# Kernel optimization log

Measured on AMD Instinct MI355X. Metric: run time of the kernel, lower is better.

## Reference

```python
import jax, jax.numpy as jnp
import numpy as np

B, S, E, D, OUT = 128, 128, 256, 256, 64


def setup_inputs() -> dict:
    key = jax.random.key(0)
    ks = jax.random.split(key, 10)
    w = lambda k, shp, s=0.05: (jax.random.normal(k, shp, dtype=jnp.float32) * s)
    return {
        "input_encoded": jax.random.normal(ks[0], (B, S, E), dtype=jnp.float32),
        "y_history": jax.random.normal(ks[1], (B, S, OUT), dtype=jnp.float32),
        "h0": jax.random.normal(ks[2], (B, D), dtype=jnp.float32) * 0.1,
        "c0": jax.random.normal(ks[3], (B, D), dtype=jnp.float32) * 0.1,
        "attn_W1": w(ks[4], (2 * D + E, E)),
        "attn_b1": jnp.zeros((E,), jnp.float32),
        "attn_w2": w(ks[5], (E,)),
        "attn_b2": jnp.zeros((1,), jnp.float32),
        "lstm_Wih": w(ks[6], (OUT, 4 * D)),
        "lstm_Whh": w(ks[7], (D, 4 * D)),
        "lstm_bih": jnp.zeros((4 * D,), jnp.float32),
        "lstm_bhh": jnp.zeros((4 * D,), jnp.float32),
        "fc_W": w(ks[8], (E + OUT, OUT)),
        "fc_b": jnp.zeros((OUT,), jnp.float32),
        "fc_out_W": w(ks[9], (D + E, OUT * S)),
        "fc_out_b": jnp.zeros((OUT * S,), jnp.float32),
    }


def reference(input_encoded, y_history, h0, c0, attn_W1, attn_b1, attn_w2, attn_b2,
              lstm_Wih, lstm_Whh, lstm_bih, lstm_bhh, fc_W, fc_b, fc_out_W, fc_out_b):
    # Split the attn first-layer weight according to the concat order (h, c, enc).
    Wh, Wc, We = attn_W1[:D], attn_W1[D:2 * D], attn_W1[2 * D:]
    # Encoder projection is time-invariant across decoder steps; hoist it.
    enc_proj = jnp.einsum('bse,ef->bsf', input_encoded, We)  # [B,S,E]

    def step(carry, y_t):
        h, c, _ = carry
        hc = h @ Wh + c @ Wc + attn_b1                       # [B,E]
        pre = jnp.tanh(enc_proj + hc[:, None, :])            # [B,S,E]
        scores = pre @ attn_w2 + attn_b2[0]                  # [B,S]
        alpha = jax.nn.softmax(scores, axis=1)
        context = jnp.einsum('bs,bse->be', alpha, input_encoded)  # [B,E]
        y_tilde = jnp.concatenate([context, y_t], axis=1) @ fc_W + fc_b  # [B,OUT]
        gates = y_tilde @ lstm_Wih + lstm_bih + h @ lstm_Whh + lstm_bhh  # [B,4D]
        i, f, g, o = jnp.split(gates, 4, axis=1)  # pytorch gate order i,f,g,o
        c_new = jax.nn.sigmoid(f) * c + jax.nn.sigmoid(i) * jnp.tanh(g)
        h_new = jax.nn.sigmoid(o) * jnp.tanh(c_new)
        return (h_new, c_new, context), None

    y_seq = jnp.transpose(y_history, (1, 0, 2))  # [S,B,OUT]
    (h_T, c_T, context_T), _ = jax.lax.scan(step, (h0, c0, jnp.zeros((B, E), h0.dtype)), y_seq)
    out = jnp.concatenate([h_T, context_T], axis=1) @ fc_out_W + fc_out_b  # [B,OUT*S]
    return out.reshape(-1, S, OUT)
```

## Files before the change

kernel.cpp:

```cpp
#include <hip/hip_runtime.h>

#define BB 128
#define SS 128
#define EE 256
#define DD 256
#define OO 64

#define W1_OFF   0
#define WHH_OFF  196608
#define WIH_OFF  458752
#define FCW_OFF  524288
#define WTOTAL   544768

__device__ __forceinline__ float fsig(float x) { return 1.0f / (1.0f + __expf(-x)); }
__device__ __forceinline__ float ftanh(float x) {
    float t = __expf(-2.0f * fabsf(x));
    float r = (1.0f - t) / (1.0f + t);
    return copysignf(r, x);
}
__device__ __forceinline__ int SWZ(int e) { return (e & ~31) | ((e + 4 * (e >> 5)) & 31); }

__device__ __forceinline__ void fma8(const uint4 w, const float xv, float* acc) {
    acc[0] += xv * __uint_as_float(w.x << 16);
    acc[1] += xv * __uint_as_float(w.x & 0xffff0000u);
    acc[2] += xv * __uint_as_float(w.y << 16);
    acc[3] += xv * __uint_as_float(w.y & 0xffff0000u);
    acc[4] += xv * __uint_as_float(w.z << 16);
    acc[5] += xv * __uint_as_float(w.z & 0xffff0000u);
    acc[6] += xv * __uint_as_float(w.w << 16);
    acc[7] += xv * __uint_as_float(w.w & 0xffff0000u);
}

__global__ __launch_bounds__(256) void conv_kernel(
    const float* __restrict__ W1, const float* __restrict__ Whh,
    const float* __restrict__ Wih, const float* __restrict__ fcW,
    unsigned short* __restrict__ out)
{
    const int idx = blockIdx.x * 256 + threadIdx.x;
    float f;
    if      (idx < WHH_OFF)  f = W1[idx];
    else if (idx < WIH_OFF)  f = Whh[idx - WHH_OFF];
    else if (idx < FCW_OFF)  f = Wih[idx - WIH_OFF];
    else if (idx < WTOTAL)   f = fcW[idx - FCW_OFF];
    else return;
    unsigned int u = __float_as_uint(f);
    u = (u + 0x7fffu + ((u >> 16) & 1u)) >> 16;
    out[idx] = (unsigned short)u;
}

__global__ __launch_bounds__(1024, 4) void scan_kernel(
    const float* __restrict__ inp,
    const float* __restrict__ yhist,
    const float* __restrict__ h0, const float* __restrict__ c0,
    const float* __restrict__ W1f,
    const float* __restrict__ b1, const float* __restrict__ w2, const float* __restrict__ b2,
    const float* __restrict__ bih, const float* __restrict__ bhh,
    const float* __restrict__ fcb,
    const unsigned short* __restrict__ wbf,
    float* __restrict__ hctxT)
{
    __shared__ float sh_h[DD], sh_c[DD], sh_hc[EE];
    __shared__ float sh_gh[1024];
    __shared__ float sh_w2[EE];
    __shared__ float sh_b1[EE], sh_bs[1024];
    __shared__ float sh_raw[SS];
    __shared__ float sh_ctx[EE], sh_y[OO], sh_yt[OO], sh_fcb[OO];
    __shared__ float sh_misc[1];
    __shared__ float red1[32 * 256];
    __shared__ float red2[8 * 1024];

    const int b = blockIdx.x, t = threadIdx.x;
    const float* inp_b = inp + b * SS * EE;
    const unsigned short* W1bf  = wbf + W1_OFF;
    const unsigned short* Whhbf = wbf + WHH_OFF;
    const unsigned short* Wihbf = wbf + WIH_OFF;
    const unsigned short* fcWbf = wbf + FCW_OFF;
    const float b2v = b2[0];

    const int e8  = (t & 31) * 8,  kc1 = t >> 5;
    const int j8  = (t & 127) * 8, kc2 = t >> 7;
    const int s_own = t >> 3,      a2  = t & 7, e0 = a2 * 32;
    const int e4  = (t & 63) * 4,  sc  = t >> 6;
    const int o4  = (t & 15) * 4,  kc3 = t >> 4;

    if (t < 256) {
        sh_h[t] = h0[b * 256 + t]; sh_c[t] = c0[b * 256 + t];
        sh_b1[t] = b1[t];
        sh_w2[SWZ(t)] = w2[t];
    }
    if (t < 64) sh_fcb[t] = fcb[t];
    sh_bs[t] = bih[t] + bhh[t];

    float er[32];
    #pragma unroll
    for (int j = 0; j < 32; ++j) er[j] = 0.f;
    {
        const float* We = W1f + 512 * 256;
        for (int kc = 0; kc < 16; ++kc) {
            {
                const int row = t >> 6, c4 = (t & 63) * 4;
                float4 v = *(const float4*)(We + (size_t)(kc * 16 + row) * 256 + c4);
                *(float4*)&red1[row * 256 + c4] = v;
            }
            {
                const int s = t >> 3, k2 = (t & 7) * 2;
                float2 v = *(const float2*)(inp_b + s * 256 + kc * 16 + k2);
                red1[4096 + s * 16 + k2] = v.x;
                red1[4096 + s * 16 + k2 + 1] = v.y;
            }
            __syncthreads();
            for (int k = 0; k < 16; ++k) {
                const float xv = red1[4096 + s_own * 16 + k];
                #pragma unroll
                for (int j4 = 0; j4 < 8; ++j4) {
                    float4 w = *(const float4*)&red1[k * 256 + e0 + j4 * 4];
                    er[j4*4+0] += xv * w.x; er[j4*4+1] += xv * w.y;
                    er[j4*4+2] += xv * w.z; er[j4*4+3] += xv * w.w;
                }
            }
            __syncthreads();
        }
    }

    for (int ts = 0; ts < SS; ++ts) {
        if (t < 64) sh_y[t] = yhist[b * SS * OO + ts * OO + t];

        {
            float acc[8];
            #pragma unroll
            for (int r = 0; r < 8; ++r) acc[r] = 0.f;
            #pragma unroll 4
            for (int k = kc1 * 16; k < kc1 * 16 + 16; ++k) {
                const float xv = (k < 256) ? sh_h[k] : sh_c[k - 256];
                uint4 w = *(const uint4*)(W1bf + (size_t)k * 256 + e8);
                fma8(w, xv, acc);
            }
            *(float4*)&red1[kc1 * 256 + e8]     = make_float4(acc[0], acc[1], acc[2], acc[3]);
            *(float4*)&red1[kc1 * 256 + e8 + 4] = make_float4(acc[4], acc[5], acc[6], acc[7]);
        }
        {
            float acc[8];
            #pragma unroll
            for (int r = 0; r < 8; ++r) acc[r] = 0.f;
            #pragma unroll 4
            for (int k = kc2 * 32; k < kc2 * 32 + 32; ++k) {
                const float hv = sh_h[k];
                uint4 w = *(const uint4*)(Whhbf + (size_t)k * 1024 + j8);
                fma8(w, hv, acc);
            }
            *(float4*)&red2[kc2 * 1024 + j8]     = make_float4(acc[0], acc[1], acc[2], acc[3]);
            *(float4*)&red2[kc2 * 1024 + j8 + 4] = make_float4(acc[4], acc[5], acc[6], acc[7]);
        }
        __syncthreads();
        if (t < 256) {
            float v = sh_b1[t];
            #pragma unroll 8
            for (int kc = 0; kc < 32; ++kc) v += red1[kc * 256 + t];
            sh_hc[SWZ(t)] = v;
        }
        {
            float v = 0.f;
            #pragma unroll
            for (int kc = 0; kc < 8; ++kc) v += red2[kc * 1024 + t];
            sh_gh[t] = v;
        }
        __syncthreads();

        {
            float acc = 0.f;
            #pragma unroll
            for (int j4 = 0; j4 < 8; ++j4) {
                const int phys = e0 + ((j4 * 4 + 4 * a2) & 31);
                float4 hc4 = *(const float4*)&sh_hc[phys];
                float4 w24 = *(const float4*)&sh_w2[phys];
                acc += ftanh(er[j4*4+0] + hc4.x) * w24.x;
                acc += ftanh(er[j4*4+1] + hc4.y) * w24.y;
                acc += ftanh(er[j4*4+2] + hc4.z) * w24.z;
                acc += ftanh(er[j4*4+3] + hc4.w) * w24.w;
            }
            acc += __shfl_xor(acc, 1);
            acc += __shfl_xor(acc, 2);
            acc += __shfl_xor(acc, 4);
            if (a2 == 0) sh_raw[s_own] = __expf(acc + b2v);
        }
        __syncthreads();
        if (t < 64) {
            float v = sh_raw[t] + sh_raw[t + 64];
            #pragma unroll
            for (int m = 32; m > 0; m >>= 1) v += __shfl_xor(v, m);
            if (t == 0) sh_misc[0] = 1.0f / v;
        }
        __syncthreads();

        {
            float ax = 0.f, ay = 0.f, az = 0.f, aw = 0.f;
            for (int s = sc * 8; s < sc * 8 + 8; ++s) {
                const float al = sh_raw[s];
                float4 iv = *(const float4*)(inp_b + s * 256 + e4);
                ax += al * iv.x; ay += al * iv.y; az += al * iv.z; aw += al * iv.w;
            }
            *(float4*)&red1[sc * 256 + e4] = make_float4(ax, ay, az, aw);
        }
        __syncthreads();
        if (t < 256) {
            float v = 0.f;
            #pragma unroll
            for (int k = 0; k < 16; ++k) v += red1[k * 256 + t];
            v *= sh_misc[0];
            sh_ctx[t] = v;
            if (ts == SS - 1) hctxT[(size_t)(256 + t) * 128 + b] = v;
        }
        __syncthreads();

        {
            float acc[4] = {0.f, 0.f, 0.f, 0.f};
            for (int kk = kc3 * 5; kk < kc3 * 5 + 5; ++kk) {
                const float val = (kk < 256) ? sh_ctx[kk] : sh_y[kk - 256];
                uint2 w = *(const uint2*)(fcWbf + kk * 64 + o4);
                acc[0] += val * __uint_as_float(w.x << 16);
                acc[1] += val * __uint_as_float(w.x & 0xffff0000u);
                acc[2] += val * __uint_as_float(w.y << 16);
                acc[3] += val * __uint_as_float(w.y & 0xffff0000u);
            }
            *(float4*)&red1[kc3 * 64 + o4] = make_float4(acc[0], acc[1], acc[2], acc[3]);
        }
        __syncthreads();
        if (t < 64) {
            float v = sh_fcb[t];
            #pragma unroll 16
            for (int kc = 0; kc < 64; ++kc) v += red1[kc * 64 + t];
            sh_yt[t] = v;
        }
        __syncthreads();

        {
            float acc[8];
            #pragma unroll
            for (int r = 0; r < 8; ++r) acc[r] = 0.f;
            #pragma unroll
            for (int k = kc2 * 8; k < kc2 * 8 + 8; ++k) {
                const float yv = sh_yt[k];
                uint4 w = *(const uint4*)(Wihbf + (size_t)k * 1024 + j8);
                fma8(w, yv, acc);
            }
            *(float4*)&red2[kc2 * 1024 + j8]     = make_float4(acc[0], acc[1], acc[2], acc[3]);
            *(float4*)&red2[kc2 * 1024 + j8 + 4] = make_float4(acc[4], acc[5], acc[6], acc[7]);
        }
        __syncthreads();
        {
            float v = sh_gh[t] + sh_bs[t];
            #pragma unroll
            for (int kc = 0; kc < 8; ++kc) v += red2[kc * 1024 + t];
            red1[t] = v;
        }
        __syncthreads();
        if (t < 256) {
            const float gi = red1[t], gf = red1[256 + t], gg = red1[512 + t], go = red1[768 + t];
            const float cn = fsig(gf) * sh_c[t] + fsig(gi) * ftanh(gg);
            sh_c[t] = cn;
            const float hn = fsig(go) * ftanh(cn);
            sh_h[t] = hn;
            if (ts == SS - 1) hctxT[(size_t)t * 128 + b] = hn;
        }
        __syncthreads();
    }
}

__global__ __launch_bounds__(256) void out_gemm(
    const float* __restrict__ AT, const float* __restrict__ W,
    const float* __restrict__ bias, float* __restrict__ out)
{
    __shared__ float Ab[64 * 132];
    __shared__ float Bb[64 * 32];
    const int t = threadIdx.x;
    const int nt = blockIdx.x * 32;
    const int n4 = (t & 7) * 4;
    const int m4 = (t >> 3) * 4;
    float acc[4][4];
    #pragma unroll
    for (int i = 0; i < 4; ++i)
        #pragma unroll
        for (int jj = 0; jj < 4; ++jj) acc[i][jj] = 0.f;

    for (int kc = 0; kc < 8; ++kc) {
        #pragma unroll
        for (int i = 0; i < 8; ++i) {
            const int flat4 = i * 256 + t;
            const int row = flat4 >> 5, mm4 = (flat4 & 31) * 4;
            float4 v = *(const float4*)(AT + (size_t)(kc * 64 + row) * 128 + mm4);
            *(float4*)&Ab[row * 132 + mm4] = v;
        }
        #pragma unroll
        for (int i = 0; i < 2; ++i) {
            const int fl = t + i * 256;
            const int k = fl >> 3, nn4 = (fl & 7) * 4;
            *(float4*)&Bb[k * 32 + nn4] =
                *(const float4*)(W + (size_t)(kc * 64 + k) * 8192 + nt + nn4);
        }
        __syncthreads();
        for (int k = 0; k < 64; ++k) {
            const float4 bv = *(const float4*)&Bb[k * 32 + n4];
            const float4 av = *(const float4*)&Ab[k * 132 + m4];
            acc[0][0] += av.x * bv.x; acc[0][1] += av.x * bv.y; acc[0][2] += av.x * bv.z; acc[0][3] += av.x * bv.w;
            acc[1][0] += av.y * bv.x; acc[1][1] += av.y * bv.y; acc[1][2] += av.y * bv.z; acc[1][3] += av.y * bv.w;
            acc[2][0] += av.z * bv.x; acc[2][1] += av.z * bv.y; acc[2][2] += av.z * bv.z; acc[2][3] += av.z * bv.w;
            acc[3][0] += av.w * bv.x; acc[3][1] += av.w * bv.y; acc[3][2] += av.w * bv.z; acc[3][3] += av.w * bv.w;
        }
        __syncthreads();
    }
    const float4 bb = *(const float4*)(bias + nt + n4);
    #pragma unroll
    for (int i = 0; i < 4; ++i) {
        float4 r;
        r.x = acc[i][0] + bb.x; r.y = acc[i][1] + bb.y;
        r.z = acc[i][2] + bb.z; r.w = acc[i][3] + bb.w;
        *(float4*)(out + (size_t)(m4 + i) * 8192 + nt + n4) = r;
    }
}

extern "C" void kernel_launch(void* const* d_in, const int* in_sizes, int n_in,
                              void* d_out, int out_size, void* d_ws, size_t ws_size,
                              hipStream_t stream) {
    const float* inp = (const float*)d_in[0];
    const float* yh  = (const float*)d_in[1];
    const float* h0  = (const float*)d_in[2];
    const float* c0  = (const float*)d_in[3];
    const float* W1  = (const float*)d_in[4];
    const float* b1  = (const float*)d_in[5];
    const float* w2  = (const float*)d_in[6];
    const float* b2  = (const float*)d_in[7];
    const float* Wih = (const float*)d_in[8];
    const float* Whh = (const float*)d_in[9];
    const float* bih = (const float*)d_in[10];
    const float* bhh = (const float*)d_in[11];
    const float* fcW = (const float*)d_in[12];
    const float* fcb = (const float*)d_in[13];
    const float* foW = (const float*)d_in[14];
    const float* fob = (const float*)d_in[15];

    float* hctxT = (float*)d_ws;
    unsigned short* wbf = (unsigned short*)d_out;

    conv_kernel<<<dim3((WTOTAL + 255) / 256), dim3(256), 0, stream>>>(W1, Whh, Wih, fcW, wbf);
    scan_kernel<<<dim3(BB), dim3(1024), 0, stream>>>(
        inp, yh, h0, c0, W1, b1, w2, b2, bih, bhh, fcb, wbf, hctxT);
    out_gemm<<<dim3(8192 / 32), dim3(256), 0, stream>>>(hctxT, foW, fob, (float*)d_out);
}
```

Before: 4.857 ms.

## Stage encoder inputs and y history in LDS as bf16, keep biases in registers

The per-block input_encoded slice (128x256) and the y_history slice are converted to bf16 and staged in shared memory once before the scan. The context reduction at each of the 128 steps then reads from LDS instead of re-reading fp32 global memory. Biases and the Whh gate partials move from shared arrays into registers. This adds about 80KB of LDS per block and bf16 rounding of the inputs in the context and fc computations, which changes numerics.

```diff
diff --git a/kernel.cpp b/kernel.cpp
--- a/kernel.cpp
+++ b/kernel.cpp
@@ -19,6 +19,12 @@
     return copysignf(r, x);
 }
 __device__ __forceinline__ int SWZ(int e) { return (e & ~31) | ((e + 4 * (e >> 5)) & 31); }
+
+__device__ __forceinline__ unsigned short bf16r(float f) {
+    unsigned int u = __float_as_uint(f);
+    u = (u + 0x7fffu + ((u >> 16) & 1u)) >> 16;
+    return (unsigned short)u;
+}
 
 __device__ __forceinline__ void fma8(const uint4 w, const float xv, float* acc) {
     acc[0] += xv * __uint_as_float(w.x << 16);
@@ -43,9 +49,7 @@
     else if (idx < FCW_OFF)  f = Wih[idx - WIH_OFF];
     else if (idx < WTOTAL)   f = fcW[idx - FCW_OFF];
     else return;
-    unsigned int u = __float_as_uint(f);
-    u = (u + 0x7fffu + ((u >> 16) & 1u)) >> 16;
-    out[idx] = (unsigned short)u;
+    out[idx] = bf16r(f);
 }
 
 __global__ __launch_bounds__(1024, 4) void scan_kernel(
@@ -60,23 +64,28 @@
     float* __restrict__ hctxT)
 {
     __shared__ float sh_h[DD], sh_c[DD], sh_hc[EE];
-    __shared__ float sh_gh[1024];
     __shared__ float sh_w2[EE];
-    __shared__ float sh_b1[EE], sh_bs[1024];
     __shared__ float sh_raw[SS];
-    __shared__ float sh_ctx[EE], sh_y[OO], sh_yt[OO], sh_fcb[OO];
+    __shared__ float sh_ctx[EE], sh_yt[OO];
     __shared__ float sh_misc[1];
     __shared__ float red1[32 * 256];
     __shared__ float red2[8 * 1024];
+    __shared__ unsigned short sh_inp[SS * EE];
+    __shared__ unsigned short sh_yh[SS * OO];
 
     const int b = blockIdx.x, t = threadIdx.x;
     const float* inp_b = inp + b * SS * EE;
+    const float* yh_b  = yhist + b * SS * OO;
     const unsigned short* W1bf  = wbf + W1_OFF;
     const unsigned short* Whhbf = wbf + WHH_OFF;
     const unsigned short* Wihbf = wbf + WIH_OFF;
     const unsigned short* fcWbf = wbf + FCW_OFF;
     const float b2v = b2[0];
 
+    const float bs_reg  = bih[t] + bhh[t];
+    const float b1_reg  = (t < 256) ? b1[t] : 0.f;
+    const float fcb_reg = (t < 64) ? fcb[t] : 0.f;
+
     const int e8  = (t & 31) * 8,  kc1 = t >> 5;
     const int j8  = (t & 127) * 8, kc2 = t >> 7;
     const int s_own = t >> 3,      a2  = t & 7, e0 = a2 * 32;
@@ -85,11 +94,25 @@
 
     if (t < 256) {
         sh_h[t] = h0[b * 256 + t]; sh_c[t] = c0[b * 256 + t];
-        sh_b1[t] = b1[t];
         sh_w2[SWZ(t)] = w2[t];
     }
-    if (t < 64) sh_fcb[t] = fcb[t];
-    sh_bs[t] = bih[t] + bhh[t];
+
+    #pragma unroll
+    for (int i = 0; i < 8; ++i) {
+        const int idx4 = t + i * 1024;
+        float4 v = *(const float4*)(inp_b + idx4 * 4);
+        unsigned int p0 = (unsigned int)bf16r(v.x) | ((unsigned int)bf16r(v.y) << 16);
+        unsigned int p1 = (unsigned int)bf16r(v.z) | ((unsigned int)bf16r(v.w) << 16);
+        *(uint2*)&sh_inp[idx4 * 4] = make_uint2(p0, p1);
+    }
+    #pragma unroll
+    for (int i = 0; i < 2; ++i) {
+        const int idx4 = t + i * 1024;
+        float4 v = *(const float4*)(yh_b + idx4 * 4);
+        unsigned int p0 = (unsigned int)bf16r(v.x) | ((unsigned int)bf16r(v.y) << 16);
+        unsigned int p1 = (unsigned int)bf16r(v.z) | ((unsigned int)bf16r(v.w) << 16);
+        *(uint2*)&sh_yh[idx4 * 4] = make_uint2(p0, p1);
+    }
 
     float er[32];
     #pragma unroll
@@ -122,9 +145,8 @@
         }
     }
 
+    float gh_reg;
     for (int ts = 0; ts < SS; ++ts) {
-        if (t < 64) sh_y[t] = yhist[b * SS * OO + ts * OO + t];
-
         {
             float acc[8];
             #pragma unroll
@@ -153,7 +175,7 @@
         }
         __syncthreads();
         if (t < 256) {
-            float v = sh_b1[t];
+            float v = b1_reg;
             #pragma unroll 8
             for (int kc = 0; kc < 32; ++kc) v += red1[kc * 256 + t];
             sh_hc[SWZ(t)] = v;
@@ -162,7 +184,7 @@
             float v = 0.f;
             #pragma unroll
             for (int kc = 0; kc < 8; ++kc) v += red2[kc * 1024 + t];
-            sh_gh[t] = v;
+            gh_reg = v;
         }
         __syncthreads();
 
@@ -196,8 +218,11 @@
             float ax = 0.f, ay = 0.f, az = 0.f, aw = 0.f;
             for (int s = sc * 8; s < sc * 8 + 8; ++s) {
                 const float al = sh_raw[s];
-                float4 iv = *(const float4*)(inp_b + s * 256 + e4);
-                ax += al * iv.x; ay += al * iv.y; az += al * iv.z; aw += al * iv.w;
+                uint2 w = *(const uint2*)&sh_inp[s * 256 + e4];
+                ax += al * __uint_as_float(w.x << 16);
+                ay += al * __uint_as_float(w.x & 0xffff0000u);
+                az += al * __uint_as_float(w.y << 16);
+                aw += al * __uint_as_float(w.y & 0xffff0000u);
             }
             *(float4*)&red1[sc * 256 + e4] = make_float4(ax, ay, az, aw);
         }
@@ -215,7 +240,9 @@
         {
             float acc[4] = {0.f, 0.f, 0.f, 0.f};
             for (int kk = kc3 * 5; kk < kc3 * 5 + 5; ++kk) {
-                const float val = (kk < 256) ? sh_ctx[kk] : sh_y[kk - 256];
+                const float val = (kk < 256)
+                    ? sh_ctx[kk]
+                    : __uint_as_float((unsigned int)sh_yh[ts * 64 + (kk - 256)] << 16);
                 uint2 w = *(const uint2*)(fcWbf + kk * 64 + o4);
                 acc[0] += val * __uint_as_float(w.x << 16);
                 acc[1] += val * __uint_as_float(w.x & 0xffff0000u);
@@ -226,7 +253,7 @@
         }
         __syncthreads();
         if (t < 64) {
-            float v = sh_fcb[t];
+            float v = fcb_reg;
             #pragma unroll 16
             for (int kc = 0; kc < 64; ++kc) v += red1[kc * 64 + t];
             sh_yt[t] = v;
@@ -248,7 +275,7 @@
         }
         __syncthreads();
         {
-            float v = sh_gh[t] + sh_bs[t];
+            float v = gh_reg + bs_reg;
             #pragma unroll
             for (int kc = 0; kc < 8; ++kc) v += red2[kc * 1024 + t];
             red1[t] = v;
```

After: 5.103 ms. 1.05x slower.

## Stream recurrent weights through double-buffered LDS via async global-to-LDS loads

Applied to the files above, without the earlier changes.

Replaces the per-step direct global reads of the W1[h,c] and Whh bf16 weights with 64KB chunks loaded by global_load_lds into two LDS buffers. Each chunk's load is issued while the previous chunk is consumed, so weight fetch overlaps compute. Reduction buffers and biases are shrunk and moved into registers. This adds twelve block-wide barriers per timestep and about 150KB of LDS, which limits the block to one per CU.

```diff
diff --git a/kernel.cpp b/kernel.cpp
--- a/kernel.cpp
+++ b/kernel.cpp
@@ -20,15 +20,18 @@
 }
 __device__ __forceinline__ int SWZ(int e) { return (e & ~31) | ((e + 4 * (e >> 5)) & 31); }
 
-__device__ __forceinline__ void fma8(const uint4 w, const float xv, float* acc) {
-    acc[0] += xv * __uint_as_float(w.x << 16);
-    acc[1] += xv * __uint_as_float(w.x & 0xffff0000u);
-    acc[2] += xv * __uint_as_float(w.y << 16);
-    acc[3] += xv * __uint_as_float(w.y & 0xffff0000u);
-    acc[4] += xv * __uint_as_float(w.z << 16);
-    acc[5] += xv * __uint_as_float(w.z & 0xffff0000u);
-    acc[6] += xv * __uint_as_float(w.w << 16);
-    acc[7] += xv * __uint_as_float(w.w & 0xffff0000u);
+__device__ __forceinline__ unsigned short bf16r(float f) {
+    unsigned int u = __float_as_uint(f);
+    u = (u + 0x7fffu + ((u >> 16) & 1u)) >> 16;
+    return (unsigned short)u;
+}
+__device__ __forceinline__ float bflo(unsigned int x) { return __uint_as_float(x << 16); }
+__device__ __forceinline__ float bfhi(unsigned int x) { return __uint_as_float(x & 0xffff0000u); }
+
+__device__ __forceinline__ void dma16(const unsigned short* g, unsigned short* l) {
+    __builtin_amdgcn_global_load_lds(
+        (const __attribute__((address_space(1))) unsigned int*)g,
+        (__attribute__((address_space(3))) unsigned int*)l, 16, 0, 0);
 }
 
 __global__ __launch_bounds__(256) void conv_kernel(
@@ -43,9 +46,7 @@
     else if (idx < FCW_OFF)  f = Wih[idx - WIH_OFF];
     else if (idx < WTOTAL)   f = fcW[idx - FCW_OFF];
     else return;
-    unsigned int u = __float_as_uint(f);
-    u = (u + 0x7fffu + ((u >> 16) & 1u)) >> 16;
-    out[idx] = (unsigned short)u;
+    out[idx] = bf16r(f);
 }
 
 __global__ __launch_bounds__(1024, 4) void scan_kernel(
@@ -59,124 +60,148 @@
     const unsigned short* __restrict__ wbf,
     float* __restrict__ hctxT)
 {
+    __shared__ unsigned short buf[2][32768];
+    __shared__ float red[5152];
     __shared__ float sh_h[DD], sh_c[DD], sh_hc[EE];
-    __shared__ float sh_gh[1024];
     __shared__ float sh_w2[EE];
-    __shared__ float sh_b1[EE], sh_bs[1024];
     __shared__ float sh_raw[SS];
-    __shared__ float sh_ctx[EE], sh_y[OO], sh_yt[OO], sh_fcb[OO];
-    __shared__ float sh_misc[1];
-    __shared__ float red1[32 * 256];
-    __shared__ float red2[8 * 1024];
+    __shared__ float sh_ctx[EE], sh_yt[OO], sh_y[OO];
 
     const int b = blockIdx.x, t = threadIdx.x;
+    const int lane = t & 63, wv = t >> 6;
     const float* inp_b = inp + b * SS * EE;
-    const unsigned short* W1bf  = wbf + W1_OFF;
-    const unsigned short* Whhbf = wbf + WHH_OFF;
     const unsigned short* Wihbf = wbf + WIH_OFF;
     const unsigned short* fcWbf = wbf + FCW_OFF;
     const float b2v = b2[0];
 
-    const int e8  = (t & 31) * 8,  kc1 = t >> 5;
-    const int j8  = (t & 127) * 8, kc2 = t >> 7;
+    const float bs_reg  = bih[t] + bhh[t];
+    const float b1_reg  = (t < 256) ? b1[t] : 0.f;
+    const float fcb_reg = (t < 64) ? fcb[t] : 0.f;
+
+    const int e4p = (t & 63) * 4,  kc1 = t >> 6;
+    const int j4  = (t & 255) * 4, kcb = t >> 8;
     const int s_own = t >> 3,      a2  = t & 7, e0 = a2 * 32;
     const int e4  = (t & 63) * 4,  sc  = t >> 6;
     const int o4  = (t & 15) * 4,  kc3 = t >> 4;
 
     if (t < 256) {
         sh_h[t] = h0[b * 256 + t]; sh_c[t] = c0[b * 256 + t];
-        sh_b1[t] = b1[t];
         sh_w2[SWZ(t)] = w2[t];
     }
-    if (t < 64) sh_fcb[t] = fcb[t];
-    sh_bs[t] = bih[t] + bhh[t];
 
     float er[32];
     #pragma unroll
     for (int j = 0; j < 32; ++j) er[j] = 0.f;
     {
+        float* stg = (float*)&buf[0][0];
         const float* We = W1f + 512 * 256;
         for (int kc = 0; kc < 16; ++kc) {
             {
                 const int row = t >> 6, c4 = (t & 63) * 4;
                 float4 v = *(const float4*)(We + (size_t)(kc * 16 + row) * 256 + c4);
-                *(float4*)&red1[row * 256 + c4] = v;
+                *(float4*)&stg[row * 256 + c4] = v;
             }
             {
                 const int s = t >> 3, k2 = (t & 7) * 2;
                 float2 v = *(const float2*)(inp_b + s * 256 + kc * 16 + k2);
-                red1[4096 + s * 16 + k2] = v.x;
-                red1[4096 + s * 16 + k2 + 1] = v.y;
+                stg[4096 + s * 16 + k2]     = v.x;
+                stg[4096 + s * 16 + k2 + 1] = v.y;
             }
             __syncthreads();
             for (int k = 0; k < 16; ++k) {
-                const float xv = red1[4096 + s_own * 16 + k];
+                const float xv = stg[4096 + s_own * 16 + k];
                 #pragma unroll
-                for (int j4 = 0; j4 < 8; ++j4) {
-                    float4 w = *(const float4*)&red1[k * 256 + e0 + j4 * 4];
-                    er[j4*4+0] += xv * w.x; er[j4*4+1] += xv * w.y;
-                    er[j4*4+2] += xv * w.z; er[j4*4+3] += xv * w.w;
+                for (int j4i = 0; j4i < 8; ++j4i) {
+                    float4 w = *(const float4*)&stg[k * 256 + e0 + j4i * 4];
+                    er[j4i*4+0] += xv * w.x; er[j4i*4+1] += xv * w.y;
+                    er[j4i*4+2] += xv * w.z; er[j4i*4+3] += xv * w.w;
                 }
             }
             __syncthreads();
         }
     }
+
+    #pragma unroll
+    for (int q = 0; q < 4; ++q) {
+        const int r1k = q * 16 + wv;
+        dma16(wbf + (size_t)r1k * 512 + lane * 8, &buf[0][r1k * 512]);
+    }
+    __syncthreads();
 
     for (int ts = 0; ts < SS; ++ts) {
         if (t < 64) sh_y[t] = yhist[b * SS * OO + ts * OO + t];
 
-        {
-            float acc[8];
-            #pragma unroll
-            for (int r = 0; r < 8; ++r) acc[r] = 0.f;
-            #pragma unroll 4
-            for (int k = kc1 * 16; k < kc1 * 16 + 16; ++k) {
-                const float xv = (k < 256) ? sh_h[k] : sh_c[k - 256];
-                uint4 w = *(const uint4*)(W1bf + (size_t)k * 256 + e8);
-                fma8(w, xv, acc);
-            }
-            *(float4*)&red1[kc1 * 256 + e8]     = make_float4(acc[0], acc[1], acc[2], acc[3]);
-            *(float4*)&red1[kc1 * 256 + e8 + 4] = make_float4(acc[4], acc[5], acc[6], acc[7]);
-        }
-        {
-            float acc[8];
-            #pragma unroll
-            for (int r = 0; r < 8; ++r) acc[r] = 0.f;
-            #pragma unroll 4
-            for (int k = kc2 * 32; k < kc2 * 32 + 32; ++k) {
-                const float hv = sh_h[k];
-                uint4 w = *(const uint4*)(Whhbf + (size_t)k * 1024 + j8);
-                fma8(w, hv, acc);
-            }
-            *(float4*)&red2[kc2 * 1024 + j8]     = make_float4(acc[0], acc[1], acc[2], acc[3]);
-            *(float4*)&red2[kc2 * 1024 + j8 + 4] = make_float4(acc[4], acc[5], acc[6], acc[7]);
-        }
-        __syncthreads();
-        if (t < 256) {
-            float v = sh_b1[t];
-            #pragma unroll 8
-            for (int kc = 0; kc < 32; ++kc) v += red1[kc * 256 + t];
-            sh_hc[SWZ(t)] = v;
-        }
-        {
-            float v = 0.f;
-            #pragma unroll
-            for (int kc = 0; kc < 8; ++kc) v += red2[kc * 1024 + t];
-            sh_gh[t] = v;
-        }
-        __syncthreads();
-
+        float acc1[4] = {0.f, 0.f, 0.f, 0.f};
+        for (int m = 0; m < 4; ++m) {
+            {
+                const size_t src = (m < 3) ? (size_t)(m + 1) * 32768 : (size_t)WHH_OFF;
+                const int pb = (m + 1) & 1;
+                #pragma unroll
+                for (int q = 0; q < 4; ++q) {
+                    const int r1k = q * 16 + wv;
+                    dma16(wbf + src + (size_t)r1k * 512 + lane * 8, &buf[pb][r1k * 512]);
+                }
+            }
+            const unsigned short* base = &buf[m & 1][0];
+            #pragma unroll
+            for (int i = 0; i < 8; ++i) {
+                const int kloc = kc1 * 8 + i;
+                const int kglob = m * 128 + kloc;
+                const float xv = (kglob < 256) ? sh_h[kglob] : sh_c[kglob - 256];
+                uint2 wvv = *(const uint2*)(base + kloc * 256 + e4p);
+                acc1[0] += xv * bflo(wvv.x); acc1[1] += xv * bfhi(wvv.x);
+                acc1[2] += xv * bflo(wvv.y); acc1[3] += xv * bfhi(wvv.y);
+            }
+            if (m == 3)
+                *(float4*)&red[kc1 * 256 + e4p] = make_float4(acc1[0], acc1[1], acc1[2], acc1[3]);
+            __syncthreads();
+        }
+
+        float acc2[4] = {0.f, 0.f, 0.f, 0.f};
+        for (int n = 0; n < 8; ++n) {
+            {
+                const size_t src = (n < 7) ? (size_t)WHH_OFF + (size_t)(n + 1) * 32768 : 0;
+                const int pb = (n + 1) & 1;
+                #pragma unroll
+                for (int q = 0; q < 4; ++q) {
+                    const int r1k = q * 16 + wv;
+                    dma16(wbf + src + (size_t)r1k * 512 + lane * 8, &buf[pb][r1k * 512]);
+                }
+            }
+            if (n == 0 && t < 256) {
+                float v = b1_reg;
+                #pragma unroll
+                for (int kc = 0; kc < 16; ++kc) v += red[kc * 256 + t];
+                sh_hc[SWZ(t)] = v;
+            }
+            const unsigned short* base = &buf[n & 1][0];
+            #pragma unroll
+            for (int i = 0; i < 8; ++i) {
+                const int kloc = kcb * 8 + i;
+                const float xv = sh_h[n * 32 + kloc];
+                uint2 wvv = *(const uint2*)(base + kloc * 1024 + j4);
+                acc2[0] += xv * bflo(wvv.x); acc2[1] += xv * bfhi(wvv.x);
+                acc2[2] += xv * bflo(wvv.y); acc2[3] += xv * bfhi(wvv.y);
+            }
+            if (n == 7)
+                *(float4*)&red[kcb * 1024 + j4] = make_float4(acc2[0], acc2[1], acc2[2], acc2[3]);
+            __syncthreads();
+        }
+
+        float gh_reg = 0.f;
+        #pragma unroll
+        for (int kc = 0; kc < 4; ++kc) gh_reg += red[kc * 1024 + t];
         {
             float acc = 0.f;
             #pragma unroll
-            for (int j4 = 0; j4 < 8; ++j4) {
-                const int phys = e0 + ((j4 * 4 + 4 * a2) & 31);
+            for (int j4i = 0; j4i < 8; ++j4i) {
+                const int phys = e0 + ((j4i * 4 + 4 * a2) & 31);
                 float4 hc4 = *(const float4*)&sh_hc[phys];
                 float4 w24 = *(const float4*)&sh_w2[phys];
-                acc += ftanh(er[j4*4+0] + hc4.x) * w24.x;
-                acc += ftanh(er[j4*4+1] + hc4.y) * w24.y;
-                acc += ftanh(er[j4*4+2] + hc4.z) * w24.z;
-                acc += ftanh(er[j4*4+3] + hc4.w) * w24.w;
+                acc += ftanh(er[j4i*4+0] + hc4.x) * w24.x;
+                acc += ftanh(er[j4i*4+1] + hc4.y) * w24.y;
+                acc += ftanh(er[j4i*4+2] + hc4.z) * w24.z;
+                acc += ftanh(er[j4i*4+3] + hc4.w) * w24.w;
             }
             acc += __shfl_xor(acc, 1);
             acc += __shfl_xor(acc, 2);
@@ -188,7 +213,7 @@
             float v = sh_raw[t] + sh_raw[t + 64];
             #pragma unroll
             for (int m = 32; m > 0; m >>= 1) v += __shfl_xor(v, m);
-            if (t == 0) sh_misc[0] = 1.0f / v;
+            if (t == 0) red[5120] = 1.0f / v;
         }
         __syncthreads();
 
@@ -199,14 +224,14 @@
                 float4 iv = *(const float4*)(inp_b + s * 256 + e4);
                 ax += al * iv.x; ay += al * iv.y; az += al * iv.z; aw += al * iv.w;
             }
-            *(float4*)&red1[sc * 256 + e4] = make_float4(ax, ay, az, aw);
+            *(float4*)&red[sc * 256 + e4] = make_float4(ax, ay, az, aw);
         }
         __syncthreads();
         if (t < 256) {
             float v = 0.f;
             #pragma unroll
-            for (int k = 0; k < 16; ++k) v += red1[k * 256 + t];
-            v *= sh_misc[0];
+            for (int k = 0; k < 16; ++k) v += red[k * 256 + t];
+            v *= red[5120];
             sh_ctx[t] = v;
             if (ts == SS - 1) hctxT[(size_t)(256 + t) * 128 + b] = v;
         }
@@ -217,45 +242,43 @@
             for (int kk = kc3 * 5; kk < kc3 * 5 + 5; ++kk) {
                 const float val = (kk < 256) ? sh_ctx[kk] : sh_y[kk - 256];
                 uint2 w = *(const uint2*)(fcWbf + kk * 64 + o4);
-                acc[0] += val * __uint_as_float(w.x << 16);
-                acc[1] += val * __uint_as_float(w.x & 0xffff0000u);
-                acc[2] += val * __uint_as_float(w.y << 16);
-                acc[3] += val * __uint_as_float(w.y & 0xffff0000u);
-            }
-            *(float4*)&red1[kc3 * 64 + o4] = make_float4(acc[0], acc[1], acc[2], acc[3]);
+                acc[0] += val * bflo(w.x); acc[1] += val * bfhi(w.x);
+                acc[2] += val * bflo(w.y); acc[3] += val * bfhi(w.y);
+            }
+            *(float4*)&red[kc3 * 64 + o4] = make_float4(acc[0], acc[1], acc[2], acc[3]);
         }
         __syncthreads();
         if (t < 64) {
-            float v = sh_fcb[t];
+            float v = fcb_reg;
             #pragma unroll 16
-            for (int kc = 0; kc < 64; ++kc) v += red1[kc * 64 + t];
+            for (int kc = 0; kc < 64; ++kc) v += red[kc * 64 + t];
             sh_yt[t] = v;
         }
         __syncthreads();
 
         {
-            float acc[8];
-            #pragma unroll
-            for (int r = 0; r < 8; ++r) acc[r] = 0.f;
-            #pragma unroll
-            for (int k = kc2 * 8; k < kc2 * 8 + 8; ++k) {
+            float acc[4] = {0.f, 0.f, 0.f, 0.f};
+            #pragma unroll 4
+            for (int k = kcb * 16; k < kcb * 16 + 16; ++k) {
                 const float yv = sh_yt[k];
-                uint4 w = *(const uint4*)(Wihbf + (size_t)k * 1024 + j8);
-                fma8(w, yv, acc);
-            }
-            *(float4*)&red2[kc2 * 1024 + j8]     = make_float4(acc[0], acc[1], acc[2], acc[3]);
-            *(float4*)&red2[kc2 * 1024 + j8 + 4] = make_float4(acc[4], acc[5], acc[6], acc[7]);
-        }
-        __syncthreads();
-        {
-            float v = sh_gh[t] + sh_bs[t];
-            #pragma unroll
-            for (int kc = 0; kc < 8; ++kc) v += red2[kc * 1024 + t];
-            red1[t] = v;
+                uint2 w = *(const uint2*)(Wihbf + (size_t)k * 1024 + j4);
+                acc[0] += yv * bflo(w.x); acc[1] += yv * bfhi(w.x);
+                acc[2] += yv * bflo(w.y); acc[3] += yv * bfhi(w.y);
+            }
+            *(float4*)&red[kcb * 1024 + j4] = make_float4(acc[0], acc[1], acc[2], acc[3]);
+        }
+        __syncthreads();
+
+        {
+            float v = gh_reg + bs_reg;
+            #pragma unroll
+            for (int kc = 0; kc < 4; ++kc) v += red[kc * 1024 + t];
+            red[4096 + t] = v;
         }
         __syncthreads();
         if (t < 256) {
-            const float gi = red1[t], gf = red1[256 + t], gg = red1[512 + t], go = red1[768 + t];
+            const float gi = red[4096 + t],       gf = red[4096 + 256 + t];
+            const float gg = red[4096 + 512 + t], go = red[4096 + 768 + t];
             const float cn = fsig(gf) * sh_c[t] + fsig(gi) * ftanh(gg);
             sh_c[t] = cn;
             const float hn = fsig(go) * ftanh(cn);
```

Result: slower. 6.181 ms (+27.3%).
